# Kernel optimization log

Measured on AMD Instinct MI355X. Metric: run time of the kernel, lower is better.

The kernel has to match this reference:

```python
import jax, jax.numpy as jnp
import numpy as np
import math

L, D_T, D, NL, NH, FFN, C, B = 24, 1024, 256, 12, 4, 1024, 2, 2048
HD = D // NH


def _layernorm(x, g, b, eps=1e-5):
    m = jnp.mean(x, axis=-1, keepdims=True)
    v = jnp.mean(jnp.square(x - m), axis=-1, keepdims=True)
    return (x - m) * jax.lax.rsqrt(v + eps) * g + b


def _rotate_half(x):
    x1, x2 = jnp.split(x, 2, axis=-1)
    return jnp.concatenate([-x2, x1], axis=-1)


def setup_inputs() -> dict:
    key = jax.random.key(0)
    ks = iter(jax.random.split(key, 64))
    n = lambda shape, s=0.02: jax.random.normal(next(ks), shape, dtype=jnp.float32) * s
    inp = {}
    inp['teacher_cls'] = jax.random.normal(next(ks), (B, L, D_T), dtype=jnp.float32)
    # input LN + projection
    inp['in_ln_g'] = jnp.ones((D_T,), jnp.float32); inp['in_ln_b'] = jnp.zeros((D_T,), jnp.float32)
    inp['proj_w'] = n((D, D_T)); inp['proj_b'] = jnp.zeros((D,), jnp.float32)
    # RoPE caches (buffers)
    inv_freq = 1.0 / (10000.0 ** (np.arange(0, D, 2, dtype=np.float32) / D))
    t = np.arange(L, dtype=np.float32)
    freqs = np.einsum('i,j->ij', t, inv_freq)
    emb = np.concatenate([freqs, freqs], axis=-1)
    inp['cos_cached'] = jnp.asarray(np.cos(emb)[None])  # [1,L,D]
    inp['sin_cached'] = jnp.asarray(np.sin(emb)[None])
    inp['pre_ln_g'] = jnp.ones((D,), jnp.float32); inp['pre_ln_b'] = jnp.zeros((D,), jnp.float32)
    # stacked transformer layer params [NL, ...]
    inp['l_ln1_g'] = jnp.ones((NL, D), jnp.float32); inp['l_ln1_b'] = jnp.zeros((NL, D), jnp.float32)
    inp['l_inw'] = n((NL, 3 * D, D)); inp['l_inb'] = jnp.zeros((NL, 3 * D), jnp.float32)
    inp['l_outw'] = n((NL, D, D)); inp['l_outb'] = jnp.zeros((NL, D), jnp.float32)
    inp['l_ln2_g'] = jnp.ones((NL, D), jnp.float32); inp['l_ln2_b'] = jnp.zeros((NL, D), jnp.float32)
    inp['l_w12'] = n((NL, 2 * FFN, D)); inp['l_b12'] = jnp.zeros((NL, 2 * FFN), jnp.float32)
    inp['l_w3'] = n((NL, D, FFN)); inp['l_b3'] = jnp.zeros((NL, D), jnp.float32)
    inp['post_ln_g'] = jnp.ones((D,), jnp.float32); inp['post_ln_b'] = jnp.zeros((D,), jnp.float32)
    # entropy gate
    inp['eg_w1'] = n((L, D, 8), 0.01); inp['eg_b1'] = jnp.zeros((L, 8), jnp.float32)
    inp['eg_w2'] = n((L, 8, 1), 0.01); inp['eg_b2'] = jnp.zeros((L, 1), jnp.float32)
    # per-position heads (stacked)
    inp['halt_w'] = n((L, D + 1)); inp['halt_b'] = jnp.full((L,), -4.0, jnp.float32)
    inp['cls_w'] = n((L, C, D)); inp['cls_b'] = jnp.zeros((L, C), jnp.float32)
    return inp


def _mha(x, inw, inb, outw, outb, mask):
    Bb, Ll, Dd = x.shape
    qkv = x @ inw.T + inb                              # [B,L,3D]
    q, k, v = jnp.split(qkv, 3, axis=-1)
    def heads(t):
        return t.reshape(Bb, Ll, NH, HD).transpose(0, 2, 1, 3)  # [B,H,L,hd]
    q, k, v = heads(q), heads(k), heads(v)
    scores = jnp.einsum('bhqd,bhkd->bhqk', q, k) / math.sqrt(HD)
    scores = jnp.where(mask, -jnp.inf, scores)
    attn = jax.nn.softmax(scores, axis=-1)
    o = jnp.einsum('bhqk,bhkd->bhqd', attn, v)
    o = o.transpose(0, 2, 1, 3).reshape(Bb, Ll, Dd)
    return o @ outw.T + outb


def reference(teacher_cls, in_ln_g, in_ln_b, proj_w, proj_b, cos_cached, sin_cached,
              pre_ln_g, pre_ln_b, l_ln1_g, l_ln1_b, l_inw, l_inb, l_outw, l_outb,
              l_ln2_g, l_ln2_b, l_w12, l_b12, l_w3, l_b3, post_ln_g, post_ln_b,
              eg_w1, eg_b1, eg_w2, eg_b2, halt_w, halt_b, cls_w, cls_b):
    x = _layernorm(teacher_cls, in_ln_g, in_ln_b)
    x = x @ proj_w.T + proj_b                          # [B,L,D]
    x = x * cos_cached + _rotate_half(x) * sin_cached  # RoPE
    z = _layernorm(x, pre_ln_g, pre_ln_b)
    mask = jnp.triu(jnp.ones((L, L), bool), 1)         # causal
    for i in range(NL):
        xn = _layernorm(z, l_ln1_g[i], l_ln1_b[i])
        z = z + _mha(xn, l_inw[i], l_inb[i], l_outw[i], l_outb[i], mask)
        xn = _layernorm(z, l_ln2_g[i], l_ln2_b[i])
        w12_out = xn @ l_w12[i].T + l_b12[i]           # [B,L,2*FFN]
        x1, x2 = jnp.split(w12_out, 2, axis=-1)
        hidden = jax.nn.silu(x1) * x2
        z = z + hidden @ l_w3[i].T + l_b3[i]
    z = _layernorm(z, post_ln_g, post_ln_b)
    # batched per-position classifier heads
    class_logits = jnp.einsum('bld,lcd->blc', z, cls_w) + cls_b   # [B,L,C]
    log_probs = jax.nn.log_softmax(class_logits, axis=-1)
    probs = jnp.exp(log_probs)
    probs_safe = jnp.clip(probs, 1e-10, 1.0)
    ent = -jnp.sum(probs_safe * jnp.log(probs_safe), axis=-1, keepdims=True)
    ent_norm = jnp.clip(ent / math.log(C), 0.0, 1.0)              # [B,L,1]
    # entropy gate
    h = jnp.tanh(jnp.einsum('bld,ldh->blh', z, eg_w1) + eg_b1)
    gate = jax.nn.sigmoid(jnp.einsum('blh,lho->blo', h, eg_w2) + eg_b2)
    gated = ent_norm * gate                                        # [B,L,1]
    # batched per-position halting heads
    combined = jnp.concatenate([z, gated], axis=-1)                # [B,L,D+1]
    halting_logits = jnp.einsum('bld,ld->bl', combined, halt_w) + halt_b
    return (halting_logits, class_logits, z)
```

## Files before the change

kernel.cpp:

```cpp
#include <hip/hip_runtime.h>
#include <hip/hip_bf16.h>
#include <math.h>

#define L_SEQ 24
#define DT 1024
#define DM 256
#define NLAYER 12
#define NHEAD 4
#define HDIM 64
#define FFND 1024
#define NCLS 2
#define NBATCH 2048
#define NTOK (NBATCH*L_SEQ)

typedef float f32x4 __attribute__((ext_vector_type(4)));
typedef __bf16 bf16x4 __attribute__((ext_vector_type(4)));
typedef __bf16 bf16x8 __attribute__((ext_vector_type(8)));

#define GLDS16(gp, lp) __builtin_amdgcn_global_load_lds((const __attribute__((address_space(1))) void*)(gp), (__attribute__((address_space(3))) void*)(lp), 16, 0, 0)
#define VMWAIT(N) asm volatile("s_waitcnt vmcnt(" #N ")" ::: "memory")
#define LGKM0()   asm volatile("s_waitcnt lgkmcnt(0)" ::: "memory")

__device__ inline float wred_sum(float v){
#pragma unroll
  for (int o = 32; o > 0; o >>= 1) v += __shfl_xor(v, o);
  return v;
}
__device__ inline float wred_max(float v){
#pragma unroll
  for (int o = 32; o > 0; o >>= 1) v = fmaxf(v, __shfl_xor(v, o));
  return v;
}

__device__ __forceinline__ void stage16x32(const __bf16* __restrict__ g, int ldk, int k0,
                                           __bf16* ldsbase, int lane, int rowbase){
  int r = rowbase + (lane >> 2);
  int cs = (lane & 3) ^ ((lane >> 3) & 3);
  GLDS16(g + (size_t)r*ldk + k0 + cs*8, ldsbase);
}
__device__ __forceinline__ bf16x8 frag32(const __bf16* tile, int row, int lane){
  int p = (lane >> 4) ^ ((row >> 1) & 3);
  return *(const bf16x8*)(tile + (row << 5) + (p << 3));
}

__device__ __forceinline__ int xcd_work(){
  int nwg = gridDim.x, bid = blockIdx.x;
  return (bid & 7) * (nwg >> 3) + (bid >> 3);
}

__global__ void cvt_bf16_kernel(const float* __restrict__ in, __bf16* __restrict__ out, int n4){
  int i = blockIdx.x * blockDim.x + threadIdx.x;
  int stride = gridDim.x * blockDim.x;
  for (; i < n4; i += stride){
    float4 v = ((const float4*)in)[i];
    bf16x4 o;
    o[0] = (__bf16)v.x; o[1] = (__bf16)v.y; o[2] = (__bf16)v.z; o[3] = (__bf16)v.w;
    ((bf16x4*)out)[i] = o;
  }
}

__global__ __launch_bounds__(256) void ln1024_kernel(
    const float* __restrict__ in, const float* __restrict__ g, const float* __restrict__ bb,
    __bf16* __restrict__ out){
  int row = blockIdx.x;
  int tid = threadIdx.x, wid = tid >> 6, lane = tid & 63;
  float4 x = ((const float4*)(in + (size_t)row*DT))[tid];
  float s = x.x + x.y + x.z + x.w;
  float q = x.x*x.x + x.y*x.y + x.z*x.z + x.w*x.w;
  s = wred_sum(s); q = wred_sum(q);
  __shared__ float red[8];
  if (lane == 0){ red[wid] = s; red[4+wid] = q; }
  __syncthreads();
  s = red[0]+red[1]+red[2]+red[3];
  q = red[4]+red[5]+red[6]+red[7];
  float mean = s * (1.f/DT);
  float rstd = rsqrtf(q*(1.f/DT) - mean*mean + 1e-5f);
  float4 gv = ((const float4*)g)[tid], bv = ((const float4*)bb)[tid];
  bf16x4 o;
  o[0] = (__bf16)((x.x-mean)*rstd*gv.x + bv.x);
  o[1] = (__bf16)((x.y-mean)*rstd*gv.y + bv.y);
  o[2] = (__bf16)((x.z-mean)*rstd*gv.z + bv.z);
  o[3] = (__bf16)((x.w-mean)*rstd*gv.w + bv.w);
  ((bf16x4*)(out + (size_t)row*DT))[tid] = o;
}

__global__ __launch_bounds__(256) void rope_preln_kernel(
    float* __restrict__ z, const float* __restrict__ cosc, const float* __restrict__ sinc,
    const float* __restrict__ g, const float* __restrict__ bb,
    const float* __restrict__ g1, const float* __restrict__ b1, __bf16* __restrict__ xnb){
  int row = blockIdx.x*4 + (threadIdx.x >> 6);
  int lane = threadIdx.x & 63;
  int l = row % L_SEQ;
  float4 x = ((const float4*)(z + (size_t)row*DM))[lane];
  float4 p;
  p.x = __shfl_xor(x.x, 32); p.y = __shfl_xor(x.y, 32);
  p.z = __shfl_xor(x.z, 32); p.w = __shfl_xor(x.w, 32);
  float sgn = (lane < 32) ? -1.f : 1.f;
  float4 c = ((const float4*)(cosc + l*DM))[lane];
  float4 sn = ((const float4*)(sinc + l*DM))[lane];
  float4 xr;
  xr.x = x.x*c.x + sgn*p.x*sn.x;
  xr.y = x.y*c.y + sgn*p.y*sn.y;
  xr.z = x.z*c.z + sgn*p.z*sn.z;
  xr.w = x.w*c.w + sgn*p.w*sn.w;
  float s = wred_sum(xr.x + xr.y + xr.z + xr.w);
  float q = wred_sum(xr.x*xr.x + xr.y*xr.y + xr.z*xr.z + xr.w*xr.w);
  float mean = s * (1.f/DM);
  float rstd = rsqrtf(q*(1.f/DM) - mean*mean + 1e-5f);
  float4 gv = ((const float4*)g)[lane], bv = ((const float4*)bb)[lane];
  float4 y;
  y.x = (xr.x-mean)*rstd*gv.x + bv.x;
  y.y = (xr.y-mean)*rstd*gv.y + bv.y;
  y.z = (xr.z-mean)*rstd*gv.z + bv.z;
  y.w = (xr.w-mean)*rstd*gv.w + bv.w;
  ((float4*)(z + (size_t)row*DM))[lane] = y;
  float s2 = wred_sum(y.x + y.y + y.z + y.w);
  float q2 = wred_sum(y.x*y.x + y.y*y.y + y.z*y.z + y.w*y.w);
  float mean2 = s2 * (1.f/DM);
  float rstd2 = rsqrtf(q2*(1.f/DM) - mean2*mean2 + 1e-5f);
  float4 g1v = ((const float4*)g1)[lane], b1v = ((const float4*)b1)[lane];
  bf16x4 o;
  o[0] = (__bf16)((y.x-mean2)*rstd2*g1v.x + b1v.x);
  o[1] = (__bf16)((y.y-mean2)*rstd2*g1v.y + b1v.y);
  o[2] = (__bf16)((y.z-mean2)*rstd2*g1v.z + b1v.z);
  o[3] = (__bf16)((y.w-mean2)*rstd2*g1v.w + b1v.w);
  ((bf16x4*)(xnb + (size_t)row*DM))[lane] = o;
}

template<int MODE, int K>
__global__ __launch_bounds__(512) void gemm512_kernel(
    const __bf16* __restrict__ A, const __bf16* __restrict__ W,
    const float* __restrict__ bias,
    float* __restrict__ Cf, __bf16* __restrict__ Cb,
    int N, int nt){
  __shared__ __align__(16) __bf16 As[2][256*32];
  __shared__ __align__(16) __bf16 Bs[2][256*32];
  int work = xcd_work();
  int bm = work / nt, bn = work % nt;
  int wid = threadIdx.x >> 6, lane = threadIdx.x & 63;
  int wr = wid >> 1, wc = wid & 1;
  int li = lane & 15, g4 = (lane >> 4) << 2;
  f32x4 acc[8][4] = {};
  const __bf16* ga = A + (size_t)bm*256*K;
  const __bf16* gb = W + (size_t)bn*256*K;
  const int NT = K/32;
  auto STAGE = [&](int b, int t){
    int k0 = t*32;
    if (wid < 4){
#pragma unroll
      for (int j = 0; j < 4; j++){ int r = (wid*4 + j)*16; stage16x32(ga, K, k0, &As[b][r<<5], lane, r); }
    } else {
#pragma unroll
      for (int j = 0; j < 4; j++){ int r = ((wid-4)*4 + j)*16; stage16x32(gb, K, k0, &Bs[b][r<<5], lane, r); }
    }
  };
  STAGE(0, 0);
  STAGE(1, 1);
  int cur = 0;
  for (int t = 0; t < NT; t++){
    if (t + 1 < NT) { VMWAIT(4); } else { VMWAIT(0); }
    __builtin_amdgcn_s_barrier();
    bf16x8 xf[4], wf[8];
#pragma unroll
    for (int mi = 0; mi < 4; mi++) xf[mi] = frag32(As[cur], wr*64 + mi*16 + li, lane);
#pragma unroll
    for (int ni = 0; ni < 8; ni++) wf[ni] = frag32(Bs[cur], wc*128 + ni*16 + li, lane);
    LGKM0();
    __builtin_amdgcn_sched_barrier(0);
    __builtin_amdgcn_s_barrier();
    if (t + 2 < NT) STAGE(cur, t+2);
    __builtin_amdgcn_s_setprio(1);
#pragma unroll
    for (int ni = 0; ni < 8; ni++)
#pragma unroll
      for (int mi = 0; mi < 4; mi++)
        acc[ni][mi] = __builtin_amdgcn_mfma_f32_16x16x32_bf16(wf[ni], xf[mi], acc[ni][mi], 0, 0, 0);
    __builtin_amdgcn_s_setprio(0);
    cur ^= 1;
  }
#pragma unroll
  for (int mi = 0; mi < 4; mi++){
    int m = bm*256 + wr*64 + mi*16 + li;
#pragma unroll
    for (int ni = 0; ni < 8; ni++){
      int n = bn*256 + wc*128 + ni*16 + g4;
      f32x4 bv = *(const f32x4*)(bias + n);
      f32x4 o = acc[ni][mi] + bv;
      if (MODE == 0){
        *(f32x4*)(Cf + (size_t)m*N + n) = o;
      } else {
        bf16x4 ob;
        ob[0] = (__bf16)o[0]; ob[1] = (__bf16)o[1]; ob[2] = (__bf16)o[2]; ob[3] = (__bf16)o[3];
        *(bf16x4*)(Cb + (size_t)m*N + n) = ob;
      }
    }
  }
}

__global__ __launch_bounds__(512) void gemm_glu_kernel(
    const __bf16* __restrict__ A, const __bf16* __restrict__ W12,
    const float* __restrict__ bias, __bf16* __restrict__ H){
  __shared__ __align__(16) __bf16 As[2][256*32];
  __shared__ __align__(16) __bf16 B1s[2][128*32];
  __shared__ __align__(16) __bf16 B2s[2][128*32];
  const int K = 256;
  int work = xcd_work();
  int bm = work >> 3, bn = work & 7;
  int wid = threadIdx.x >> 6, lane = threadIdx.x & 63;
  int wr = wid >> 1, wc = wid & 1;
  int li = lane & 15, g4 = (lane >> 4) << 2;
  f32x4 acc1[4][4] = {}, acc2[4][4] = {};
  const __bf16* ga  = A   + (size_t)bm*256*K;
  const __bf16* gb1 = W12 + (size_t)bn*128*K;
  const __bf16* gb2 = gb1 + (size_t)1024*K;
  auto STAGE = [&](int b, int t){
    int k0 = t*32;
    if (wid < 4){
#pragma unroll
      for (int j = 0; j < 4; j++){ int r = (wid*4 + j)*16; stage16x32(ga, K, k0, &As[b][r<<5], lane, r); }
    } else if (wid < 6){
#pragma unroll
      for (int j = 0; j < 4; j++){ int r = ((wid-4)*4 + j)*16; stage16x32(gb1, K, k0, &B1s[b][r<<5], lane, r); }
    } else {
#pragma unroll
      for (int j = 0; j < 4; j++){ int r = ((wid-6)*4 + j)*16; stage16x32(gb2, K, k0, &B2s[b][r<<5], lane, r); }
    }
  };
  STAGE(0, 0);
  STAGE(1, 1);
  int cur = 0;
  for (int t = 0; t < 8; t++){
    if (t + 1 < 8) { VMWAIT(4); } else { VMWAIT(0); }
    __builtin_amdgcn_s_barrier();
    bf16x8 xf[4], w1f[4], w2f[4];
#pragma unroll
    for (int mi = 0; mi < 4; mi++) xf[mi] = frag32(As[cur], wr*64 + mi*16 + li, lane);
#pragma unroll
    for (int ni = 0; ni < 4; ni++){
      w1f[ni] = frag32(B1s[cur], wc*64 + ni*16 + li, lane);
      w2f[ni] = frag32(B2s[cur], wc*64 + ni*16 + li, lane);
    }
    LGKM0();
    __builtin_amdgcn_sched_barrier(0);
    __builtin_amdgcn_s_barrier();
    if (t + 2 < 8) STAGE(cur, t+2);
    __builtin_amdgcn_s_setprio(1);
#pragma unroll
    for (int ni = 0; ni < 4; ni++)
#pragma unroll
      for (int mi = 0; mi < 4; mi++){
        acc1[ni][mi] = __builtin_amdgcn_mfma_f32_16x16x32_bf16(w1f[ni], xf[mi], acc1[ni][mi], 0, 0, 0);
        acc2[ni][mi] = __builtin_amdgcn_mfma_f32_16x16x32_bf16(w2f[ni], xf[mi], acc2[ni][mi], 0, 0, 0);
      }
    __builtin_amdgcn_s_setprio(0);
    cur ^= 1;
  }
#pragma unroll
  for (int mi = 0; mi < 4; mi++){
    int m = bm*256 + wr*64 + mi*16 + li;
#pragma unroll
    for (int ni = 0; ni < 4; ni++){
      int n = bn*128 + wc*64 + ni*16 + g4;
      f32x4 b1v = *(const f32x4*)(bias + n);
      f32x4 b2v = *(const f32x4*)(bias + 1024 + n);
      bf16x4 ob;
#pragma unroll
      for (int r = 0; r < 4; r++){
        float v1 = acc1[ni][mi][r] + b1v[r];
        float v2 = acc2[ni][mi][r] + b2v[r];
        float sig = 1.f/(1.f + __expf(-v1));
        ob[r] = (__bf16)(v1*sig*v2);
      }
      *(bf16x4*)(H + (size_t)m*FFND + n) = ob;
    }
  }
}

template<int K>
__global__ __launch_bounds__(512) void gemm_ln_kernel(
    const __bf16* __restrict__ A, const __bf16* __restrict__ W,
    const float* __restrict__ bias, float* __restrict__ z,
    const float* __restrict__ lng, const float* __restrict__ lnb,
    __bf16* __restrict__ outb, float* __restrict__ outf){
  __shared__ __align__(16) __bf16 As[2][256*32];
  __shared__ __align__(16) __bf16 Bs[2][256*32];
  __shared__ float redS[256][2], redQ[256][2];
  int bm = xcd_work();
  int wid = threadIdx.x >> 6, lane = threadIdx.x & 63;
  int wr = wid >> 1, wc = wid & 1;
  int li = lane & 15, g4 = (lane >> 4) << 2;
  f32x4 acc[8][4] = {};
  const __bf16* ga = A + (size_t)bm*256*K;
  const int NT = K/32;
  auto STAGE = [&](int b, int t){
    int k0 = t*32;
    if (wid < 4){
#pragma unroll
      for (int j = 0; j < 4; j++){ int r = (wid*4 + j)*16; stage16x32(ga, K, k0, &As[b][r<<5], lane, r); }
    } else {
#pragma unroll
      for (int j = 0; j < 4; j++){ int r = ((wid-4)*4 + j)*16; stage16x32(W, K, k0, &Bs[b][r<<5], lane, r); }
    }
  };
  STAGE(0, 0);
  STAGE(1, 1);
  int cur = 0;
  for (int t = 0; t < NT; t++){
    if (t + 1 < NT) { VMWAIT(4); } else { VMWAIT(0); }
    __builtin_amdgcn_s_barrier();
    bf16x8 xf[4], wf[8];
#pragma unroll
    for (int mi = 0; mi < 4; mi++) xf[mi] = frag32(As[cur], wr*64 + mi*16 + li, lane);
#pragma unroll
    for (int ni = 0; ni < 8; ni++) wf[ni] = frag32(Bs[cur], wc*128 + ni*16 + li, lane);
    LGKM0();
    __builtin_amdgcn_sched_barrier(0);
    __builtin_amdgcn_s_barrier();
    if (t + 2 < NT) STAGE(cur, t+2);
    __builtin_amdgcn_s_setprio(1);
#pragma unroll
    for (int ni = 0; ni < 8; ni++)
#pragma unroll
      for (int mi = 0; mi < 4; mi++)
        acc[ni][mi] = __builtin_amdgcn_mfma_f32_16x16x32_bf16(wf[ni], xf[mi], acc[ni][mi], 0, 0, 0);
    __builtin_amdgcn_s_setprio(0);
    cur ^= 1;
  }
  float sA[4] = {}, qA[4] = {};
#pragma unroll
  for (int mi = 0; mi < 4; mi++){
    int m = bm*256 + wr*64 + mi*16 + li;
#pragma unroll
    for (int ni = 0; ni < 8; ni++){
      int n = wc*128 + ni*16 + g4;
      f32x4 zv = *(const f32x4*)(z + (size_t)m*DM + n);
      f32x4 bv = *(const f32x4*)(bias + n);
      f32x4 v = acc[ni][mi] + bv + zv;
      acc[ni][mi] = v;
      *(f32x4*)(z + (size_t)m*DM + n) = v;
#pragma unroll
      for (int r = 0; r < 4; r++){ sA[mi] += v[r]; qA[mi] += v[r]*v[r]; }
    }
  }
  __syncthreads();
#pragma unroll
  for (int mi = 0; mi < 4; mi++){
    float s = sA[mi], q = qA[mi];
    s += __shfl_xor(s, 16); q += __shfl_xor(q, 16);
    s += __shfl_xor(s, 32); q += __shfl_xor(q, 32);
    if (lane < 16){ redS[wr*64 + mi*16 + li][wc] = s; redQ[wr*64 + mi*16 + li][wc] = q; }
  }
  __syncthreads();
#pragma unroll
  for (int mi = 0; mi < 4; mi++){
    int ml = wr*64 + mi*16 + li;
    float s = redS[ml][0] + redS[ml][1];
    float q = redQ[ml][0] + redQ[ml][1];
    float mean = s * (1.f/DM);
    float rstd = rsqrtf(q*(1.f/DM) - mean*mean + 1e-5f);
    int m = bm*256 + ml;
#pragma unroll
    for (int ni = 0; ni < 8; ni++){
      int n = wc*128 + ni*16 + g4;
      f32x4 gv = *(const f32x4*)(lng + n);
      f32x4 bv = *(const f32x4*)(lnb + n);
      if (outb){
        bf16x4 o;
#pragma unroll
        for (int r = 0; r < 4; r++) o[r] = (__bf16)((acc[ni][mi][r] - mean)*rstd*gv[r] + bv[r]);
        *(bf16x4*)(outb + (size_t)m*DM + n) = o;
      } else {
        f32x4 o;
#pragma unroll
        for (int r = 0; r < 4; r++) o[r] = (acc[ni][mi][r] - mean)*rstd*gv[r] + bv[r];
        *(f32x4*)(outf + (size_t)m*DM + n) = o;
      }
    }
  }
}

__global__ __launch_bounds__(256) void attn_kernel(const __bf16* __restrict__ qkv, __bf16* __restrict__ ob){
  int b = blockIdx.x;
  int h = threadIdx.x >> 6, lane = threadIdx.x & 63;
  __shared__ __align__(16) __bf16 Qs[NHEAD][L_SEQ][HDIM];
  __shared__ __align__(16) __bf16 Ks[NHEAD][L_SEQ][HDIM];
  __shared__ float Ps[NHEAD][L_SEQ][L_SEQ];
  const __bf16* base = qkv + (size_t)b*L_SEQ*768;
  float V[L_SEQ];
#pragma unroll
  for (int t = 0; t < L_SEQ; t++){
    int sw = lane ^ ((t & 7) << 3);
    Qs[h][t][sw] = base[t*768 + h*64 + lane];
    Ks[h][t][sw] = base[t*768 + 256 + h*64 + lane];
    V[t] = (float)base[t*768 + 512 + h*64 + lane];
  }
  __syncthreads();
  for (int p = lane; p < L_SEQ*L_SEQ; p += 64){
    int q = p / L_SEQ, k = p - q*L_SEQ;
    if (k <= q){
      int qx = (q & 7) << 3, kx = (k & 7) << 3;
      const __bf16* qr = Qs[h][q];
      const __bf16* kr = Ks[h][k];
      float s = 0.f;
#pragma unroll
      for (int d = 0; d < 64; d += 4){
        bf16x4 qa = *(const bf16x4*)(qr + (d ^ qx));
        bf16x4 ka = *(const bf16x4*)(kr + (d ^ kx));
        s += (float)qa[0]*(float)ka[0] + (float)qa[1]*(float)ka[1]
           + (float)qa[2]*(float)ka[2] + (float)qa[3]*(float)ka[3];
      }
      Ps[h][q][k] = s * 0.125f;
    }
  }
  __syncthreads();
  for (int q = 0; q < L_SEQ; q++){
    float v = (lane <= q) ? Ps[h][q][lane] : -1e30f;
    float mx = wred_max(v);
    float e = (lane <= q) ? __expf(v - mx) : 0.f;
    float sm = wred_sum(e);
    if (lane < L_SEQ) Ps[h][q][lane] = e / sm;
  }
  __syncthreads();
  for (int q = 0; q < L_SEQ; q++){
    float o = 0.f;
    for (int k = 0; k <= q; k++) o += Ps[h][q][k] * V[k];
    ob[((size_t)b*L_SEQ + q)*DM + h*64 + lane] = (__bf16)o;
  }
}

__global__ __launch_bounds__(256) void heads_kernel(
    const float* __restrict__ z,
    const float* __restrict__ cls_w, const float* __restrict__ cls_b,
    const float* __restrict__ eg_w1, const float* __restrict__ eg_b1,
    const float* __restrict__ eg_w2, const float* __restrict__ eg_b2,
    const float* __restrict__ halt_w, const float* __restrict__ halt_b,
    float* __restrict__ halt_out, float* __restrict__ cls_out){
  int m = blockIdx.x*4 + (threadIdx.x >> 6);
  int lane = threadIdx.x & 63;
  int l = m % L_SEQ;
  float4 zv = ((const float4*)(z + (size_t)m*DM))[lane];
  float4 w0 = ((const float4*)(cls_w + ((size_t)l*2 + 0)*DM))[lane];
  float4 w1 = ((const float4*)(cls_w + ((size_t)l*2 + 1)*DM))[lane];
  float c0 = wred_sum(zv.x*w0.x + zv.y*w0.y + zv.z*w0.z + zv.w*w0.w) + cls_b[l*2 + 0];
  float c1 = wred_sum(zv.x*w1.x + zv.y*w1.y + zv.z*w1.z + zv.w*w1.w) + cls_b[l*2 + 1];
  float mx = fmaxf(c0, c1);
  float e0 = __expf(c0 - mx), e1 = __expf(c1 - mx);
  float inv = 1.f/(e0 + e1);
  float p0 = fminf(fmaxf(e0*inv, 1e-10f), 1.f);
  float p1 = fminf(fmaxf(e1*inv, 1e-10f), 1.f);
  float ent = -(p0*__logf(p0) + p1*__logf(p1));
  float entn = fminf(fmaxf(ent * 1.44269504f, 0.f), 1.f);
  const float4* wg = (const float4*)(eg_w1 + ((size_t)l*DM + 4*lane)*8);
  float hacc[8] = {};
#pragma unroll
  for (int dd = 0; dd < 4; dd++){
    float zd = (dd==0) ? zv.x : (dd==1) ? zv.y : (dd==2) ? zv.z : zv.w;
    float4 a = wg[dd*2], b = wg[dd*2 + 1];
    hacc[0] += zd*a.x; hacc[1] += zd*a.y; hacc[2] += zd*a.z; hacc[3] += zd*a.w;
    hacc[4] += zd*b.x; hacc[5] += zd*b.y; hacc[6] += zd*b.z; hacc[7] += zd*b.w;
  }
  float gin = 0.f;
#pragma unroll
  for (int j = 0; j < 8; j++){
    float hj = wred_sum(hacc[j]);
    hj = tanhf(hj + eg_b1[l*8 + j]);
    gin += hj * eg_w2[l*8 + j];
  }
  gin += eg_b2[l];
  float gate = 1.f/(1.f + __expf(-gin));
  float gated = entn * gate;
  const float* hw = halt_w + (size_t)l*257;
  float hp = zv.x*hw[4*lane] + zv.y*hw[4*lane+1] + zv.z*hw[4*lane+2] + zv.w*hw[4*lane+3];
  float hl = wred_sum(hp) + gated*hw[256] + halt_b[l];
  if (lane == 0) halt_out[m] = hl;
  if (lane < 2) cls_out[(size_t)m*2 + lane] = lane ? c1 : c0;
}

extern "C" void kernel_launch(void* const* d_in, const int* in_sizes, int n_in,
                              void* d_out, int out_size, void* d_ws, size_t ws_size,
                              hipStream_t stream){
  const float* teacher = (const float*)d_in[0];
  const float* in_ln_g = (const float*)d_in[1];
  const float* in_ln_b = (const float*)d_in[2];
  const float* proj_w  = (const float*)d_in[3];
  const float* proj_b  = (const float*)d_in[4];
  const float* cosc    = (const float*)d_in[5];
  const float* sinc    = (const float*)d_in[6];
  const float* pre_g   = (const float*)d_in[7];
  const float* pre_b   = (const float*)d_in[8];
  const float* l_ln1_g = (const float*)d_in[9];
  const float* l_ln1_b = (const float*)d_in[10];
  const float* l_inw   = (const float*)d_in[11];
  const float* l_inb   = (const float*)d_in[12];
  const float* l_outw  = (const float*)d_in[13];
  const float* l_outb  = (const float*)d_in[14];
  const float* l_ln2_g = (const float*)d_in[15];
  const float* l_ln2_b = (const float*)d_in[16];
  const float* l_w12   = (const float*)d_in[17];
  const float* l_b12   = (const float*)d_in[18];
  const float* l_w3    = (const float*)d_in[19];
  const float* l_b3    = (const float*)d_in[20];
  const float* post_g  = (const float*)d_in[21];
  const float* post_b  = (const float*)d_in[22];
  const float* eg_w1   = (const float*)d_in[23];
  const float* eg_b1   = (const float*)d_in[24];
  const float* eg_w2   = (const float*)d_in[25];
  const float* eg_b2   = (const float*)d_in[26];
  const float* halt_w  = (const float*)d_in[27];
  const float* halt_b  = (const float*)d_in[28];
  const float* cls_w   = (const float*)d_in[29];
  const float* cls_b   = (const float*)d_in[30];

  float* out = (float*)d_out;
  float* halt_out = out;
  float* cls_out  = out + NTOK;
  float* z_out    = out + NTOK + (size_t)NTOK*NCLS;

  char* ws = (char*)d_ws;
  size_t off = 0;
  auto alloc = [&](size_t bytes){ void* p = ws + off; off += (bytes + 255) & ~(size_t)255; return p; };
  float*  zbuf = (float*) alloc((size_t)NTOK*DM*4);
  __bf16* xnb  = (__bf16*)alloc((size_t)NTOK*DM*2);
  __bf16* qkvb = (__bf16*)alloc((size_t)NTOK*768*2);
  __bf16* obuf = (__bf16*)alloc((size_t)NTOK*DM*2);
  __bf16* bigb = (__bf16*)alloc((size_t)NTOK*1024*2);
  __bf16* w_proj = (__bf16*)alloc((size_t)262144*2);
  __bf16* w_in   = (__bf16*)alloc((size_t)2359296*2);
  __bf16* w_out  = (__bf16*)alloc((size_t)786432*2);
  __bf16* w_12   = (__bf16*)alloc((size_t)6291456*2);
  __bf16* w_3    = (__bf16*)alloc((size_t)3145728*2);

  cvt_bf16_kernel<<<256, 256, 0, stream>>>(proj_w, w_proj, 262144/4);
  cvt_bf16_kernel<<<1024, 256, 0, stream>>>(l_inw, w_in, 2359296/4);
  cvt_bf16_kernel<<<512, 256, 0, stream>>>(l_outw, w_out, 786432/4);
  cvt_bf16_kernel<<<2048, 256, 0, stream>>>(l_w12, w_12, 6291456/4);
  cvt_bf16_kernel<<<1024, 256, 0, stream>>>(l_w3, w_3, 3145728/4);

  ln1024_kernel<<<NTOK, 256, 0, stream>>>(teacher, in_ln_g, in_ln_b, bigb);
  gemm512_kernel<0, 1024><<<192, 512, 0, stream>>>(bigb, w_proj, proj_b, zbuf, nullptr, 256, 1);
  rope_preln_kernel<<<NTOK/4, 256, 0, stream>>>(zbuf, cosc, sinc, pre_g, pre_b, l_ln1_g, l_ln1_b, xnb);

  for (int i = 0; i < NLAYER; i++){
    gemm512_kernel<1, 256><<<576, 512, 0, stream>>>(xnb, w_in + (size_t)i*768*256, l_inb + i*768, nullptr, qkvb, 768, 3);
    attn_kernel<<<NBATCH, 256, 0, stream>>>(qkvb, obuf);
    gemm_ln_kernel<256><<<192, 512, 0, stream>>>(obuf, w_out + (size_t)i*256*256, l_outb + i*256,
                                                 zbuf, l_ln2_g + i*256, l_ln2_b + i*256, xnb, nullptr);
    gemm_glu_kernel<<<1536, 512, 0, stream>>>(xnb, w_12 + (size_t)i*2048*256, l_b12 + i*2048, bigb);
    bool last = (i == NLAYER-1);
    gemm_ln_kernel<1024><<<192, 512, 0, stream>>>(bigb, w_3 + (size_t)i*256*1024, l_b3 + i*256,
                                                  zbuf,
                                                  last ? post_g : l_ln1_g + (i+1)*256,
                                                  last ? post_b : l_ln1_b + (i+1)*256,
                                                  last ? nullptr : xnb,
                                                  last ? z_out : nullptr);
  }

  heads_kernel<<<NTOK/4, 256, 0, stream>>>(z_out, cls_w, cls_b, eg_w1, eg_b1, eg_w2, eg_b2,
                                           halt_w, halt_b, halt_out, cls_out);
}
```

Measured before the change: 3.942 ms.

## Fuse attention with out-projection GEMM, residual and LayerNorm; merge weight casts

Attention is now computed per 8-sequence block (one wave per sequence, looping over heads) with its output written straight into a swizzled LDS tile. The same block then runs the out-projection MFMA GEMM, residual add and LN2 in place, which drops the obuf round trip through global memory and one launch per layer. The five weight-cast launches are merged into one kernel. In exchange the fused kernel uses about 156KB of LDS, so occupancy is low and heads are processed serially. The grid also shrinks to 256 blocks, which is thin on a large GPU.

```diff
diff --git a/kernel.cpp b/kernel.cpp
--- a/kernel.cpp
+++ b/kernel.cpp
@@ -48,14 +48,25 @@
   return (bid & 7) * (nwg >> 3) + (bid >> 3);
 }
 
-__global__ void cvt_bf16_kernel(const float* __restrict__ in, __bf16* __restrict__ out, int n4){
-  int i = blockIdx.x * blockDim.x + threadIdx.x;
+__global__ void cvt_all_kernel(const float* __restrict__ a0, __bf16* __restrict__ o0, int n0,
+                               const float* __restrict__ a1, __bf16* __restrict__ o1, int n1,
+                               const float* __restrict__ a2, __bf16* __restrict__ o2, int n2,
+                               const float* __restrict__ a3, __bf16* __restrict__ o3, int n3,
+                               const float* __restrict__ a4, __bf16* __restrict__ o4, int n4){
   int stride = gridDim.x * blockDim.x;
-  for (; i < n4; i += stride){
-    float4 v = ((const float4*)in)[i];
-    bf16x4 o;
-    o[0] = (__bf16)v.x; o[1] = (__bf16)v.y; o[2] = (__bf16)v.z; o[3] = (__bf16)v.w;
-    ((bf16x4*)out)[i] = o;
+  int i0 = blockIdx.x * blockDim.x + threadIdx.x;
+  const float* as[5] = {a0,a1,a2,a3,a4};
+  __bf16* os[5] = {o0,o1,o2,o3,o4};
+  int ns[5] = {n0,n1,n2,n3,n4};
+#pragma unroll
+  for (int s = 0; s < 5; s++){
+    const float* a = as[s]; __bf16* o = os[s]; int n = ns[s];
+    for (int i = i0; i < n; i += stride){
+      float4 v = ((const float4*)a)[i];
+      bf16x4 ov;
+      ov[0] = (__bf16)v.x; ov[1] = (__bf16)v.y; ov[2] = (__bf16)v.z; ov[3] = (__bf16)v.w;
+      ((bf16x4*)o)[i] = ov;
+    }
   }
 }
 
@@ -379,52 +390,164 @@
   }
 }
 
-__global__ __launch_bounds__(256) void attn_kernel(const __bf16* __restrict__ qkv, __bf16* __restrict__ ob){
-  int b = blockIdx.x;
-  int h = threadIdx.x >> 6, lane = threadIdx.x & 63;
-  __shared__ __align__(16) __bf16 Qs[NHEAD][L_SEQ][HDIM];
-  __shared__ __align__(16) __bf16 Ks[NHEAD][L_SEQ][HDIM];
-  __shared__ float Ps[NHEAD][L_SEQ][L_SEQ];
-  const __bf16* base = qkv + (size_t)b*L_SEQ*768;
-  float V[L_SEQ];
-#pragma unroll
-  for (int t = 0; t < L_SEQ; t++){
-    int sw = lane ^ ((t & 7) << 3);
-    Qs[h][t][sw] = base[t*768 + h*64 + lane];
-    Ks[h][t][sw] = base[t*768 + 256 + h*64 + lane];
-    V[t] = (float)base[t*768 + 512 + h*64 + lane];
+#define O_OFF   0
+#define U_OFF   98304
+#define QK_OFF  (U_OFF)
+#define PS_OFF  (U_OFF + 49152)
+#define SM_SIZE 159744
+
+__global__ __launch_bounds__(512) void attn_proj_ln_kernel(
+    const __bf16* __restrict__ qkv, const __bf16* __restrict__ Wout,
+    const float* __restrict__ bias, float* __restrict__ z,
+    const float* __restrict__ lng, const float* __restrict__ lnb,
+    __bf16* __restrict__ xnb){
+  __shared__ __align__(16) char SM[SM_SIZE];
+  __bf16* Otile = (__bf16*)(SM + O_OFF);
+  int bm = blockIdx.x;
+  int wid = threadIdx.x >> 6, lane = threadIdx.x & 63;
+  const int ROFF[24] = {0,4,8,12,16,24,32,40,48,60,72,84,96,112,128,144,160,180,200,220,240,264,288,312};
+
+  {
+    const __bf16* base = qkv + (size_t)(bm*8 + wid)*L_SEQ*768;
+    __bf16* Qs = (__bf16*)(SM + QK_OFF + wid*6144);
+    __bf16* Ks = Qs + 24*64;
+    float*  Ps = (float*)(SM + PS_OFF + wid*1536);
+    for (int j = 0; j < NHEAD; j++){
+      float V[L_SEQ];
+#pragma unroll
+      for (int t = 0; t < L_SEQ; t++){
+        int sw = lane ^ ((t & 7) << 3);
+        Qs[t*64 + sw] = base[t*768 + j*64 + lane];
+        Ks[t*64 + sw] = base[t*768 + 256 + j*64 + lane];
+        V[t] = (float)base[t*768 + 512 + j*64 + lane];
+      }
+      __syncthreads();
+      for (int p = lane; p < L_SEQ*L_SEQ; p += 64){
+        int q = p / L_SEQ, k = p - q*L_SEQ;
+        if (k <= q){
+          int qx = (q & 7) << 3, kx = (k & 7) << 3;
+          const __bf16* qr = Qs + q*64;
+          const __bf16* kr = Ks + k*64;
+          float s = 0.f;
+#pragma unroll
+          for (int d = 0; d < 64; d += 4){
+            bf16x4 qa = *(const bf16x4*)(qr + (d ^ qx));
+            bf16x4 ka = *(const bf16x4*)(kr + (d ^ kx));
+            s += (float)qa[0]*(float)ka[0] + (float)qa[1]*(float)ka[1]
+               + (float)qa[2]*(float)ka[2] + (float)qa[3]*(float)ka[3];
+          }
+          Ps[ROFF[q] + k] = s * 0.125f;
+        }
+      }
+      __syncthreads();
+#pragma unroll
+      for (int q = 0; q < L_SEQ; q++){
+        float v = (lane <= q) ? Ps[ROFF[q] + lane] : -1e30f;
+        float mx = wred_max(v);
+        float e = (lane <= q) ? __expf(v - mx) : 0.f;
+        float sm = wred_sum(e);
+        int plen = (q + 4) & ~3;
+        if (lane <= q) Ps[ROFF[q] + lane] = e / sm;
+        else if (lane < plen) Ps[ROFF[q] + lane] = 0.f;
+      }
+      __syncthreads();
+#pragma unroll
+      for (int q = 0; q < L_SEQ; q++){
+        float o = 0.f;
+        int plen = (q + 4) & ~3;
+        for (int k0 = 0; k0 < plen; k0 += 4){
+          float4 pv = *(const float4*)&Ps[ROFF[q] + k0];
+          o += pv.x*V[k0] + pv.y*V[k0+1] + pv.z*V[k0+2] + pv.w*V[k0+3];
+        }
+        int row = wid*24 + q;
+        int col = j*64 + lane;
+        int kc = col >> 5, c = col & 31;
+        int p8 = (c >> 3) ^ ((row >> 1) & 3);
+        Otile[kc*(192*32) + row*32 + p8*8 + (c & 7)] = (__bf16)o;
+      }
+      __syncthreads();
+    }
   }
   __syncthreads();
-  for (int p = lane; p < L_SEQ*L_SEQ; p += 64){
-    int q = p / L_SEQ, k = p - q*L_SEQ;
-    if (k <= q){
-      int qx = (q & 7) << 3, kx = (k & 7) << 3;
-      const __bf16* qr = Qs[h][q];
-      const __bf16* kr = Ks[h][k];
-      float s = 0.f;
-#pragma unroll
-      for (int d = 0; d < 64; d += 4){
-        bf16x4 qa = *(const bf16x4*)(qr + (d ^ qx));
-        bf16x4 ka = *(const bf16x4*)(kr + (d ^ kx));
-        s += (float)qa[0]*(float)ka[0] + (float)qa[1]*(float)ka[1]
-           + (float)qa[2]*(float)ka[2] + (float)qa[3]*(float)ka[3];
-      }
-      Ps[h][q][k] = s * 0.125f;
+
+  __bf16* Wd = (__bf16*)(SM + U_OFF);
+  int wr = wid >> 1, wc = wid & 1;
+  int li = lane & 15, g4 = (lane >> 4) << 2;
+  f32x4 acc[8][3] = {};
+  auto STAGE = [&](int b, int t){
+    int k0 = t*32;
+    stage16x32(Wout, 256, k0, Wd + b*8192 + ((wid*32) << 5),      lane, wid*32);
+    stage16x32(Wout, 256, k0, Wd + b*8192 + ((wid*32 + 16) << 5), lane, wid*32 + 16);
+  };
+  STAGE(0, 0);
+  STAGE(1, 1);
+  int cur = 0;
+  for (int t = 0; t < 8; t++){
+    if (t + 1 < 8) { VMWAIT(2); } else { VMWAIT(0); }
+    __builtin_amdgcn_s_barrier();
+    bf16x8 xf[3], wf[8];
+#pragma unroll
+    for (int mi = 0; mi < 3; mi++) xf[mi] = frag32(Otile + t*(192*32), wr*48 + mi*16 + li, lane);
+#pragma unroll
+    for (int ni = 0; ni < 8; ni++) wf[ni] = frag32(Wd + cur*8192, wc*128 + ni*16 + li, lane);
+    LGKM0();
+    __builtin_amdgcn_sched_barrier(0);
+    __builtin_amdgcn_s_barrier();
+    if (t + 2 < 8) STAGE(cur, t+2);
+    __builtin_amdgcn_s_setprio(1);
+#pragma unroll
+    for (int ni = 0; ni < 8; ni++)
+#pragma unroll
+      for (int mi = 0; mi < 3; mi++)
+        acc[ni][mi] = __builtin_amdgcn_mfma_f32_16x16x32_bf16(wf[ni], xf[mi], acc[ni][mi], 0, 0, 0);
+    __builtin_amdgcn_s_setprio(0);
+    cur ^= 1;
+  }
+  float* redS = (float*)(SM + U_OFF + 32768);
+  float* redQ = redS + 384;
+  float sA[3] = {}, qA[3] = {};
+#pragma unroll
+  for (int mi = 0; mi < 3; mi++){
+    int m = bm*192 + wr*48 + mi*16 + li;
+#pragma unroll
+    for (int ni = 0; ni < 8; ni++){
+      int n = wc*128 + ni*16 + g4;
+      f32x4 zv = *(const f32x4*)(z + (size_t)m*DM + n);
+      f32x4 bv = *(const f32x4*)(bias + n);
+      f32x4 v = acc[ni][mi] + bv + zv;
+      acc[ni][mi] = v;
+      *(f32x4*)(z + (size_t)m*DM + n) = v;
+#pragma unroll
+      for (int r = 0; r < 4; r++){ sA[mi] += v[r]; qA[mi] += v[r]*v[r]; }
     }
   }
   __syncthreads();
-  for (int q = 0; q < L_SEQ; q++){
-    float v = (lane <= q) ? Ps[h][q][lane] : -1e30f;
-    float mx = wred_max(v);
-    float e = (lane <= q) ? __expf(v - mx) : 0.f;
-    float sm = wred_sum(e);
-    if (lane < L_SEQ) Ps[h][q][lane] = e / sm;
+#pragma unroll
+  for (int mi = 0; mi < 3; mi++){
+    float s = sA[mi], q = qA[mi];
+    s += __shfl_xor(s, 16); q += __shfl_xor(q, 16);
+    s += __shfl_xor(s, 32); q += __shfl_xor(q, 32);
+    if (lane < 16){ int rl = wr*48 + mi*16 + li; redS[rl*2 + wc] = s; redQ[rl*2 + wc] = q; }
   }
   __syncthreads();
-  for (int q = 0; q < L_SEQ; q++){
-    float o = 0.f;
-    for (int k = 0; k <= q; k++) o += Ps[h][q][k] * V[k];
-    ob[((size_t)b*L_SEQ + q)*DM + h*64 + lane] = (__bf16)o;
+#pragma unroll
+  for (int mi = 0; mi < 3; mi++){
+    int rl = wr*48 + mi*16 + li;
+    float s = redS[rl*2 + 0] + redS[rl*2 + 1];
+    float q = redQ[rl*2 + 0] + redQ[rl*2 + 1];
+    float mean = s * (1.f/DM);
+    float rstd = rsqrtf(q*(1.f/DM) - mean*mean + 1e-5f);
+    int m = bm*192 + rl;
+#pragma unroll
+    for (int ni = 0; ni < 8; ni++){
+      int n = wc*128 + ni*16 + g4;
+      f32x4 gv = *(const f32x4*)(lng + n);
+      f32x4 bv = *(const f32x4*)(lnb + n);
+      bf16x4 o;
+#pragma unroll
+      for (int r = 0; r < 4; r++) o[r] = (__bf16)((acc[ni][mi][r] - mean)*rstd*gv[r] + bv[r]);
+      *(bf16x4*)(xnb + (size_t)m*DM + n) = o;
+    }
   }
 }
 
@@ -522,7 +645,6 @@
   float*  zbuf = (float*) alloc((size_t)NTOK*DM*4);
   __bf16* xnb  = (__bf16*)alloc((size_t)NTOK*DM*2);
   __bf16* qkvb = (__bf16*)alloc((size_t)NTOK*768*2);
-  __bf16* obuf = (__bf16*)alloc((size_t)NTOK*DM*2);
   __bf16* bigb = (__bf16*)alloc((size_t)NTOK*1024*2);
   __bf16* w_proj = (__bf16*)alloc((size_t)262144*2);
   __bf16* w_in   = (__bf16*)alloc((size_t)2359296*2);
@@ -530,11 +652,11 @@
   __bf16* w_12   = (__bf16*)alloc((size_t)6291456*2);
   __bf16* w_3    = (__bf16*)alloc((size_t)3145728*2);
 
-  cvt_bf16_kernel<<<256, 256, 0, stream>>>(proj_w, w_proj, 262144/4);
-  cvt_bf16_kernel<<<1024, 256, 0, stream>>>(l_inw, w_in, 2359296/4);
-  cvt_bf16_kernel<<<512, 256, 0, stream>>>(l_outw, w_out, 786432/4);
-  cvt_bf16_kernel<<<2048, 256, 0, stream>>>(l_w12, w_12, 6291456/4);
-  cvt_bf16_kernel<<<1024, 256, 0, stream>>>(l_w3, w_3, 3145728/4);
+  cvt_all_kernel<<<2048, 256, 0, stream>>>(proj_w, w_proj, 262144/4,
+                                           l_inw, w_in, 2359296/4,
+                                           l_outw, w_out, 786432/4,
+                                           l_w12, w_12, 6291456/4,
+                                           l_w3, w_3, 3145728/4);
 
   ln1024_kernel<<<NTOK, 256, 0, stream>>>(teacher, in_ln_g, in_ln_b, bigb);
   gemm512_kernel<0, 1024><<<192, 512, 0, stream>>>(bigb, w_proj, proj_b, zbuf, nullptr, 256, 1);
@@ -542,9 +664,8 @@
 
   for (int i = 0; i < NLAYER; i++){
     gemm512_kernel<1, 256><<<576, 512, 0, stream>>>(xnb, w_in + (size_t)i*768*256, l_inb + i*768, nullptr, qkvb, 768, 3);
-    attn_kernel<<<NBATCH, 256, 0, stream>>>(qkvb, obuf);
-    gemm_ln_kernel<256><<<192, 512, 0, stream>>>(obuf, w_out + (size_t)i*256*256, l_outb + i*256,
-                                                 zbuf, l_ln2_g + i*256, l_ln2_b + i*256, xnb, nullptr);
+    attn_proj_ln_kernel<<<NBATCH/8, 512, 0, stream>>>(qkvb, w_out + (size_t)i*256*256, l_outb + i*256,
+                                                      zbuf, l_ln2_g + i*256, l_ln2_b + i*256, xnb);
     gemm_glu_kernel<<<1536, 512, 0, stream>>>(xnb, w_12 + (size_t)i*2048*256, l_b12 + i*2048, bigb);
     bool last = (i == NLAYER-1);
     gemm_ln_kernel<1024><<<192, 512, 0, stream>>>(bigb, w_3 + (size_t)i*256*1024, l_b3 + i*256,
```

Result: slower. 4.753 ms (+20.6%).

## Make GLU GEMM persistent over N with A tile resident in LDS

Applied to the files above, without the earlier changes.

The GLU GEMM now launches 256 blocks, each loading a 192-row slice of the activation once into LDS (all K chunks) and looping over all 8 output column tiles, streaming only W1/W2 tiles through a double buffer. This stops the activation tile from being reloaded once per N tile and cuts the grid from 1536 to 256 blocks. In exchange there is a larger LDS footprint, one wave of blocks on 256 CUs with no tail overlap, and per-tile epilogues inside the loop. The five weight-conversion launches are also merged into one kernel.

```diff
diff --git a/kernel.cpp b/kernel.cpp
--- a/kernel.cpp
+++ b/kernel.cpp
@@ -48,14 +48,25 @@
   return (bid & 7) * (nwg >> 3) + (bid >> 3);
 }
 
-__global__ void cvt_bf16_kernel(const float* __restrict__ in, __bf16* __restrict__ out, int n4){
-  int i = blockIdx.x * blockDim.x + threadIdx.x;
+__global__ void cvt_all_kernel(const float* __restrict__ a0, __bf16* __restrict__ o0, int n0,
+                               const float* __restrict__ a1, __bf16* __restrict__ o1, int n1,
+                               const float* __restrict__ a2, __bf16* __restrict__ o2, int n2,
+                               const float* __restrict__ a3, __bf16* __restrict__ o3, int n3,
+                               const float* __restrict__ a4, __bf16* __restrict__ o4, int n4){
   int stride = gridDim.x * blockDim.x;
-  for (; i < n4; i += stride){
-    float4 v = ((const float4*)in)[i];
-    bf16x4 o;
-    o[0] = (__bf16)v.x; o[1] = (__bf16)v.y; o[2] = (__bf16)v.z; o[3] = (__bf16)v.w;
-    ((bf16x4*)out)[i] = o;
+  int i0 = blockIdx.x * blockDim.x + threadIdx.x;
+  const float* as[5] = {a0,a1,a2,a3,a4};
+  __bf16* os[5] = {o0,o1,o2,o3,o4};
+  int ns[5] = {n0,n1,n2,n3,n4};
+#pragma unroll
+  for (int s = 0; s < 5; s++){
+    const float* a = as[s]; __bf16* o = os[s]; int n = ns[s];
+    for (int i = i0; i < n; i += stride){
+      float4 v = ((const float4*)a)[i];
+      bf16x4 ov;
+      ov[0] = (__bf16)v.x; ov[1] = (__bf16)v.y; ov[2] = (__bf16)v.z; ov[3] = (__bf16)v.w;
+      ((bf16x4*)o)[i] = ov;
+    }
   }
 }
 
@@ -200,41 +211,41 @@
 __global__ __launch_bounds__(512) void gemm_glu_kernel(
     const __bf16* __restrict__ A, const __bf16* __restrict__ W12,
     const float* __restrict__ bias, __bf16* __restrict__ H){
-  __shared__ __align__(16) __bf16 As[2][256*32];
+  __shared__ __align__(16) __bf16 As[8][192*32];
   __shared__ __align__(16) __bf16 B1s[2][128*32];
   __shared__ __align__(16) __bf16 B2s[2][128*32];
   const int K = 256;
-  int work = xcd_work();
-  int bm = work >> 3, bn = work & 7;
+  int bm = xcd_work();
   int wid = threadIdx.x >> 6, lane = threadIdx.x & 63;
   int wr = wid >> 1, wc = wid & 1;
   int li = lane & 15, g4 = (lane >> 4) << 2;
-  f32x4 acc1[4][4] = {}, acc2[4][4] = {};
-  const __bf16* ga  = A   + (size_t)bm*256*K;
-  const __bf16* gb1 = W12 + (size_t)bn*128*K;
-  const __bf16* gb2 = gb1 + (size_t)1024*K;
-  auto STAGE = [&](int b, int t){
-    int k0 = t*32;
-    if (wid < 4){
-#pragma unroll
-      for (int j = 0; j < 4; j++){ int r = (wid*4 + j)*16; stage16x32(ga, K, k0, &As[b][r<<5], lane, r); }
-    } else if (wid < 6){
-#pragma unroll
-      for (int j = 0; j < 4; j++){ int r = ((wid-4)*4 + j)*16; stage16x32(gb1, K, k0, &B1s[b][r<<5], lane, r); }
-    } else {
-#pragma unroll
-      for (int j = 0; j < 4; j++){ int r = ((wid-6)*4 + j)*16; stage16x32(gb2, K, k0, &B2s[b][r<<5], lane, r); }
-    }
+  const __bf16* ga = A + (size_t)bm*192*K;
+#pragma unroll
+  for (int j = 0; j < 12; j++){
+    int g = j*8 + wid;
+    int chunk = g / 12, u = g % 12;
+    stage16x32(ga, K, chunk*32, &As[chunk][(u*16) << 5], lane, u*16);
+  }
+  auto STAGEB = [&](int buf, int g){
+    int bn = g >> 3, k0 = (g & 7)*32;
+    const __bf16* gb1 = W12 + (size_t)bn*128*K;
+    stage16x32(gb1,              K, k0, &B1s[buf][(wid*16) << 5], lane, wid*16);
+    stage16x32(gb1 + (size_t)1024*K, K, k0, &B2s[buf][(wid*16) << 5], lane, wid*16);
   };
-  STAGE(0, 0);
-  STAGE(1, 1);
+  STAGEB(0, 0);
+  STAGEB(1, 1);
+  f32x4 acc1[4][3] = {}, acc2[4][3] = {};
   int cur = 0;
-  for (int t = 0; t < 8; t++){
-    if (t + 1 < 8) { VMWAIT(4); } else { VMWAIT(0); }
+  for (int g = 0; g < 64; g++){
+    int k = g & 7, bn = g >> 3;
+    if (g == 0)            { VMWAIT(2);  }
+    else if (g == 63)      { VMWAIT(0);  }
+    else if (k == 0)       { VMWAIT(14); }
+    else                   { VMWAIT(2);  }
     __builtin_amdgcn_s_barrier();
-    bf16x8 xf[4], w1f[4], w2f[4];
-#pragma unroll
-    for (int mi = 0; mi < 4; mi++) xf[mi] = frag32(As[cur], wr*64 + mi*16 + li, lane);
+    bf16x8 xf[3], w1f[4], w2f[4];
+#pragma unroll
+    for (int mi = 0; mi < 3; mi++) xf[mi] = frag32(As[k], wr*48 + mi*16 + li, lane);
 #pragma unroll
     for (int ni = 0; ni < 4; ni++){
       w1f[ni] = frag32(B1s[cur], wc*64 + ni*16 + li, lane);
@@ -243,35 +254,39 @@
     LGKM0();
     __builtin_amdgcn_sched_barrier(0);
     __builtin_amdgcn_s_barrier();
-    if (t + 2 < 8) STAGE(cur, t+2);
+    if (g + 2 < 64) STAGEB(cur, g + 2);
     __builtin_amdgcn_s_setprio(1);
 #pragma unroll
     for (int ni = 0; ni < 4; ni++)
 #pragma unroll
-      for (int mi = 0; mi < 4; mi++){
+      for (int mi = 0; mi < 3; mi++){
         acc1[ni][mi] = __builtin_amdgcn_mfma_f32_16x16x32_bf16(w1f[ni], xf[mi], acc1[ni][mi], 0, 0, 0);
         acc2[ni][mi] = __builtin_amdgcn_mfma_f32_16x16x32_bf16(w2f[ni], xf[mi], acc2[ni][mi], 0, 0, 0);
       }
     __builtin_amdgcn_s_setprio(0);
     cur ^= 1;
-  }
-#pragma unroll
-  for (int mi = 0; mi < 4; mi++){
-    int m = bm*256 + wr*64 + mi*16 + li;
-#pragma unroll
-    for (int ni = 0; ni < 4; ni++){
-      int n = bn*128 + wc*64 + ni*16 + g4;
-      f32x4 b1v = *(const f32x4*)(bias + n);
-      f32x4 b2v = *(const f32x4*)(bias + 1024 + n);
-      bf16x4 ob;
-#pragma unroll
-      for (int r = 0; r < 4; r++){
-        float v1 = acc1[ni][mi][r] + b1v[r];
-        float v2 = acc2[ni][mi][r] + b2v[r];
-        float sig = 1.f/(1.f + __expf(-v1));
-        ob[r] = (__bf16)(v1*sig*v2);
+    if (k == 7){
+#pragma unroll
+      for (int mi = 0; mi < 3; mi++){
+        int m = bm*192 + wr*48 + mi*16 + li;
+#pragma unroll
+        for (int ni = 0; ni < 4; ni++){
+          int n = bn*128 + wc*64 + ni*16 + g4;
+          f32x4 b1v = *(const f32x4*)(bias + n);
+          f32x4 b2v = *(const f32x4*)(bias + 1024 + n);
+          bf16x4 ob;
+#pragma unroll
+          for (int r = 0; r < 4; r++){
+            float v1 = acc1[ni][mi][r] + b1v[r];
+            float v2 = acc2[ni][mi][r] + b2v[r];
+            float sig = 1.f/(1.f + __expf(-v1));
+            ob[r] = (__bf16)(v1*sig*v2);
+          }
+          *(bf16x4*)(H + (size_t)m*FFND + n) = ob;
+          acc1[ni][mi] = (f32x4)(0.f);
+          acc2[ni][mi] = (f32x4)(0.f);
+        }
       }
-      *(bf16x4*)(H + (size_t)m*FFND + n) = ob;
     }
   }
 }
@@ -530,11 +545,11 @@
   __bf16* w_12   = (__bf16*)alloc((size_t)6291456*2);
   __bf16* w_3    = (__bf16*)alloc((size_t)3145728*2);
 
-  cvt_bf16_kernel<<<256, 256, 0, stream>>>(proj_w, w_proj, 262144/4);
-  cvt_bf16_kernel<<<1024, 256, 0, stream>>>(l_inw, w_in, 2359296/4);
-  cvt_bf16_kernel<<<512, 256, 0, stream>>>(l_outw, w_out, 786432/4);
-  cvt_bf16_kernel<<<2048, 256, 0, stream>>>(l_w12, w_12, 6291456/4);
-  cvt_bf16_kernel<<<1024, 256, 0, stream>>>(l_w3, w_3, 3145728/4);
+  cvt_all_kernel<<<2048, 256, 0, stream>>>(proj_w, w_proj, 262144/4,
+                                           l_inw, w_in, 2359296/4,
+                                           l_outw, w_out, 786432/4,
+                                           l_w12, w_12, 6291456/4,
+                                           l_w3, w_3, 3145728/4);
 
   ln1024_kernel<<<NTOK, 256, 0, stream>>>(teacher, in_ln_g, in_ln_b, bigb);
   gemm512_kernel<0, 1024><<<192, 512, 0, stream>>>(bigb, w_proj, proj_b, zbuf, nullptr, 256, 1);
@@ -545,7 +560,7 @@
     attn_kernel<<<NBATCH, 256, 0, stream>>>(qkvb, obuf);
     gemm_ln_kernel<256><<<192, 512, 0, stream>>>(obuf, w_out + (size_t)i*256*256, l_outb + i*256,
                                                  zbuf, l_ln2_g + i*256, l_ln2_b + i*256, xnb, nullptr);
-    gemm_glu_kernel<<<1536, 512, 0, stream>>>(xnb, w_12 + (size_t)i*2048*256, l_b12 + i*2048, bigb);
+    gemm_glu_kernel<<<256, 512, 0, stream>>>(xnb, w_12 + (size_t)i*2048*256, l_b12 + i*2048, bigb);
     bool last = (i == NLAYER-1);
     gemm_ln_kernel<1024><<<192, 512, 0, stream>>>(bigb, w_3 + (size_t)i*256*1024, l_b3 + i*256,
                                                   zbuf,
```

Result: slower. 4.143 ms (+5.1%).
